# Kernel tuning notes

Measured on AMD Instinct MI355X. Metric: run time of the kernel, lower is better.

## Reference

```python
import jax, jax.numpy as jnp
import numpy as np

C = 128; PE = 8; WALK = 20; NODE_F = 28; EDGE_F = 4
L = 4; H = 4; DH = C // H; B = 64; NPG = 512; N = B * NPG; E = 262144
BN_EPS = 1e-5


def _bn(x, g, b):
    # BatchNorm1d, training-mode statistics (biased var), over the node axis
    m = x.mean(0)
    v = x.var(0)
    return (x - m) * jax.lax.rsqrt(v + BN_EPS) * g + b


def _forward(pe, node_emb, pe_lin_w, pe_lin_b, pe_norm_g, pe_norm_b, edge_emb,
             gine_w1, gine_b1, gine_w2, gine_b2,
             attn_wqkv, attn_bqkv, attn_wo, attn_bo,
             norm1_g, norm1_b, norm2_g, norm2_b, norm3_g, norm3_b,
             ffn_w1, ffn_b1, ffn_w2, ffn_b2,
             mlp_w1, mlp_b1, mlp_w2, mlp_b2, mlp_w3, mlp_b3,
             x, edge_index, edge_attr, batch):
    pe_n = _bn(pe, pe_norm_g, pe_norm_b)
    h = jnp.concatenate([node_emb[x[:, 0]], pe_n @ pe_lin_w + pe_lin_b], axis=1)  # [N, C]
    ea = edge_emb[edge_attr]  # [E, C]
    src, dst = edge_index[0], edge_index[1]
    scale = 1.0 / jnp.sqrt(jnp.asarray(DH, h.dtype))
    for l in range(L):
        # --- GINEConv: nn((1+eps)*x + sum_{j->i} relu(x_j + e_ji)), eps=0 ---
        msg = jax.nn.relu(h[src] + ea)                      # [E, C] gather
        agg = jax.ops.segment_sum(msg, dst, num_segments=N) # [N, C] scatter-add
        z = agg + h
        local = jax.nn.relu(z @ gine_w1[l] + gine_b1[l]) @ gine_w2[l] + gine_b2[l]
        h_loc = _bn(local + h, norm1_g[l], norm1_b[l])
        # --- global multihead attention on dense batch [B, NPG, C] (equal-size graphs) ---
        xd = h.reshape(B, NPG, C)
        qkv = xd @ attn_wqkv[l] + attn_bqkv[l]              # [B, NPG, 3C]
        q, k, v = jnp.split(qkv, 3, axis=-1)
        q = q.reshape(B, NPG, H, DH)
        k = k.reshape(B, NPG, H, DH)
        v = v.reshape(B, NPG, H, DH)
        att = jax.nn.softmax(jnp.einsum('bqhd,bkhd->bhqk', q, k) * scale, axis=-1)
        o = jnp.einsum('bhqk,bkhd->bqhd', att, v).reshape(B, NPG, C) @ attn_wo[l] + attn_bo[l]
        h_att = _bn(o.reshape(N, C) + h, norm2_g[l], norm2_b[l])
        # --- combine + FFN (GPSConv) ---
        out = h_loc + h_att
        ffn = jax.nn.relu(out @ ffn_w1[l] + ffn_b1[l]) @ ffn_w2[l] + ffn_b2[l]
        h = _bn(out + ffn, norm3_g[l], norm3_b[l])
    g = jax.ops.segment_sum(h, batch, num_segments=B)       # global_add_pool -> [B, C]
    y = jax.nn.relu(g @ mlp_w1 + mlp_b1)
    y = jax.nn.relu(y @ mlp_w2 + mlp_b2)
    return y @ mlp_w3 + mlp_b3                              # [B, 1]


def setup_inputs() -> dict:
    key = jax.random.key(0)
    ks = iter(jax.random.split(key, 48))
    def w(shape, s=0.05):
        return jax.random.normal(next(ks), shape, jnp.float32) * s
    inp = {}
    inp['x'] = jax.random.randint(next(ks), (N, 1), 0, NODE_F)
    inp['pe'] = jax.random.normal(next(ks), (N, WALK), jnp.float32)
    inp['edge_index'] = jax.random.randint(next(ks), (2, E), 0, N)
    inp['edge_attr'] = jax.random.randint(next(ks), (E,), 0, EDGE_F)
    inp['batch'] = jnp.arange(N, dtype=jnp.int32) // NPG
    inp['node_emb'] = w((NODE_F, C - PE), 1.0)
    inp['pe_lin_w'] = w((WALK, PE))
    inp['pe_lin_b'] = jnp.zeros((PE,), jnp.float32)
    inp['pe_norm_g'] = jnp.ones((WALK,), jnp.float32)
    inp['pe_norm_b'] = jnp.zeros((WALK,), jnp.float32)
    inp['edge_emb'] = w((EDGE_F, C), 1.0)
    inp['gine_w1'] = w((L, C, C))
    inp['gine_b1'] = jnp.zeros((L, C), jnp.float32)
    inp['gine_w2'] = w((L, C, C))
    inp['gine_b2'] = jnp.zeros((L, C), jnp.float32)
    inp['attn_wqkv'] = w((L, C, 3 * C))
    inp['attn_bqkv'] = jnp.zeros((L, 3 * C), jnp.float32)
    inp['attn_wo'] = w((L, C, C))
    inp['attn_bo'] = jnp.zeros((L, C), jnp.float32)
    for nm in ('norm1', 'norm2', 'norm3'):
        inp[nm + '_g'] = jnp.ones((L, C), jnp.float32)
        inp[nm + '_b'] = jnp.zeros((L, C), jnp.float32)
    inp['ffn_w1'] = w((L, C, 2 * C))
    inp['ffn_b1'] = jnp.zeros((L, 2 * C), jnp.float32)
    inp['ffn_w2'] = w((L, 2 * C, C))
    inp['ffn_b2'] = jnp.zeros((L, C), jnp.float32)
    inp['mlp_w1'] = w((C, C // 2))
    inp['mlp_b1'] = jnp.zeros((C // 2,), jnp.float32)
    inp['mlp_w2'] = w((C // 2, C // 4))
    inp['mlp_b2'] = jnp.zeros((C // 4,), jnp.float32)
    inp['mlp_w3'] = w((C // 4, 1))
    inp['mlp_b3'] = jnp.zeros((1,), jnp.float32)
    return inp


def reference(x, pe, edge_index, edge_attr, batch,
              node_emb, pe_lin_w, pe_lin_b, pe_norm_g, pe_norm_b, edge_emb,
              gine_w1, gine_b1, gine_w2, gine_b2,
              attn_wqkv, attn_bqkv, attn_wo, attn_bo,
              norm1_g, norm1_b, norm2_g, norm2_b, norm3_g, norm3_b,
              ffn_w1, ffn_b1, ffn_w2, ffn_b2,
              mlp_w1, mlp_b1, mlp_w2, mlp_b2, mlp_w3, mlp_b3):
    return _forward(pe, node_emb, pe_lin_w, pe_lin_b, pe_norm_g, pe_norm_b, edge_emb,
                    gine_w1, gine_b1, gine_w2, gine_b2,
                    attn_wqkv, attn_bqkv, attn_wo, attn_bo,
                    norm1_g, norm1_b, norm2_g, norm2_b, norm3_g, norm3_b,
                    ffn_w1, ffn_b1, ffn_w2, ffn_b2,
                    mlp_w1, mlp_b1, mlp_w2, mlp_b2, mlp_w3, mlp_b3,
                    x, edge_index, edge_attr, batch)
```

## Files before the change

### kernel.cpp

```cpp
#include <hip/hip_runtime.h>
#include <math.h>
#include <cstddef>

#define N_NODES 32768
#define C_DIM   128
#define E_EDGES 262144
#define B_GR    64
#define NPG     512
#define WALK_D  20
#define L_LAYERS 4

static constexpr int NF = N_NODES * C_DIM;

typedef __attribute__((ext_vector_type(8))) short bf16x8;
typedef __attribute__((ext_vector_type(4))) float f32x4;
typedef __attribute__((ext_vector_type(4))) short short4v;

__device__ inline unsigned short f2bf(float f)
{
    union { float f; unsigned u; } v; v.f = f;
    unsigned r = v.u + 0x7fff + ((v.u >> 16) & 1);
    return (unsigned short)(r >> 16);
}
__device__ inline float bf2f_lo(unsigned u) { return __uint_as_float(u << 16); }
__device__ inline float bf2f_hi(unsigned u) { return __uint_as_float(u & 0xffff0000u); }

__global__ __launch_bounds__(256) void pe_stats_k(const float* __restrict__ pe, float* __restrict__ acc)
{
    int gt = blockIdx.x * 256 + threadIdx.x;
    float s[WALK_D], q[WALK_D];
    #pragma unroll
    for (int c = 0; c < WALK_D; ++c) { s[c] = 0.f; q[c] = 0.f; }
    for (int r = 0; r < 4; ++r) {
        const float* row = &pe[(size_t)(gt + r * 8192) * WALK_D];
        float v[20];
        #pragma unroll
        for (int j = 0; j < 5; ++j) *(float4*)&v[j * 4] = *(const float4*)(row + j * 4);
        #pragma unroll
        for (int c = 0; c < WALK_D; ++c) { s[c] += v[c]; q[c] += v[c] * v[c]; }
    }
    #pragma unroll
    for (int c = 0; c < WALK_D; ++c) {
        float ss = s[c], qq = q[c];
        #pragma unroll
        for (int m = 1; m < 64; m <<= 1) { ss += __shfl_xor(ss, m); qq += __shfl_xor(qq, m); }
        if ((threadIdx.x & 63) == 0) { atomicAdd(&acc[c], ss); atomicAdd(&acc[32 + c], qq); }
    }
}

__global__ void pe_fin_k(const float* __restrict__ acc, const float* __restrict__ g,
                         const float* __restrict__ b, float* __restrict__ sf)
{
    int c = threadIdx.x;
    if (c >= WALK_D) return;
    float mean = acc[c] * (1.f / N_NODES);
    float var  = acc[32 + c] * (1.f / N_NODES) - mean * mean;
    float sc   = g[c] * rsqrtf(var + 1e-5f);
    sf[c] = sc;
    sf[32 + c] = b[c] - mean * sc;
}

__global__ __launch_bounds__(256) void h0_k(const int* __restrict__ x, const float* __restrict__ pe,
    const float* __restrict__ node_emb, const float* __restrict__ plw, const float* __restrict__ plb,
    const float* __restrict__ pesf, float* __restrict__ h, unsigned short* __restrict__ h16)
{
    int tid = threadIdx.x;
    int i = blockIdx.x * 2 + (tid >> 7);
    int c = tid & 127;
    float v;
    if (c < 120) {
        v = node_emb[x[i] * 120 + c];
    } else {
        int pc = c - 120;
        v = plb[pc];
        #pragma unroll
        for (int k = 0; k < WALK_D; ++k) {
            float pn = pe[i * WALK_D + k] * pesf[k] + pesf[32 + k];
            v = fmaf(pn, plw[k * 8 + pc], v);
        }
    }
    h[i * C_DIM + c] = v;
    h16[i * C_DIM + c] = f2bf(v);
}

__global__ __launch_bounds__(256) void hist_k(const int* __restrict__ dst, int* __restrict__ cnt)
{
    int e = blockIdx.x * 256 + threadIdx.x;
    atomicAdd(&cnt[dst[e]], 1);
}

__global__ __launch_bounds__(256) void bsum_k(const int* __restrict__ cnt, int* __restrict__ bsum)
{
    __shared__ int ws[4];
    int b = blockIdx.x, t = threadIdx.x;
    int v = cnt[b * 256 + t];
    #pragma unroll
    for (int m = 1; m < 64; m <<= 1) v += __shfl_xor(v, m);
    if ((t & 63) == 0) ws[t >> 6] = v;
    __syncthreads();
    if (t == 0) bsum[b] = ws[0] + ws[1] + ws[2] + ws[3];
}

__global__ __launch_bounds__(128) void bscan_k(const int* __restrict__ bsum, int* __restrict__ bpre)
{
    __shared__ int s[128];
    int t = threadIdx.x;
    int v = bsum[t];
    s[t] = v;
    __syncthreads();
    for (int off = 1; off < 128; off <<= 1) {
        int u = (t >= off) ? s[t - off] : 0;
        __syncthreads();
        s[t] += u;
        __syncthreads();
    }
    bpre[t] = s[t] - v;
}

__global__ __launch_bounds__(256) void indptr_k(const int* __restrict__ cnt, const int* __restrict__ bpre,
                                                int* __restrict__ indptr)
{
    __shared__ int s[256];
    int b = blockIdx.x, t = threadIdx.x;
    int v = cnt[b * 256 + t];
    s[t] = v;
    __syncthreads();
    for (int off = 1; off < 256; off <<= 1) {
        int u = (t >= off) ? s[t - off] : 0;
        __syncthreads();
        s[t] += u;
        __syncthreads();
    }
    indptr[b * 256 + t] = bpre[b] + s[t] - v;
    if (b == 127 && t == 255) indptr[N_NODES] = E_EDGES;
}

__global__ __launch_bounds__(256) void scatter_k(const int* __restrict__ dst, const int* __restrict__ indptr,
                                                 int* __restrict__ cur, int* __restrict__ eid)
{
    int e = blockIdx.x * 256 + threadIdx.x;
    int d = dst[e];
    int pos = atomicAdd(&cur[d], 1);
    eid[indptr[d] + pos] = e;
}

__global__ __launch_bounds__(256) void gine_gather_k(const unsigned short* __restrict__ h16,
    const int* __restrict__ src, const int* __restrict__ attr,
    const int* __restrict__ indptr, const int* __restrict__ eid,
    const float* __restrict__ edge_emb, unsigned short* __restrict__ z16)
{
    __shared__ float ee[4 * C_DIM];
    int tid = threadIdx.x;
    ee[tid] = edge_emb[tid];
    ee[tid + 256] = edge_emb[tid + 256];
    __syncthreads();
    int i = blockIdx.x * 4 + (tid >> 6);
    int c = (tid & 63) * 2;
    int p0 = indptr[i], p1 = indptr[i + 1];
    float s0 = 0.f, s1 = 0.f;
    for (int p = p0; p < p1; ++p) {
        int e  = eid[p];
        int sv = src[e];
        int av = attr[e];
        unsigned u = *(const unsigned*)&h16[(size_t)sv * C_DIM + c];
        float m0 = bf2f_lo(u) + ee[av * C_DIM + c];
        float m1 = bf2f_hi(u) + ee[av * C_DIM + c + 1];
        s0 += fmaxf(m0, 0.f);
        s1 += fmaxf(m1, 0.f);
    }
    unsigned us = *(const unsigned*)&h16[(size_t)i * C_DIM + c];
    s0 += bf2f_lo(us);
    s1 += bf2f_hi(us);
    unsigned out = (unsigned)f2bf(s0) | ((unsigned)f2bf(s1) << 16);
    *(unsigned*)&z16[(size_t)i * C_DIM + c] = out;
}

__global__ __launch_bounds__(256) void wt_prep_k(
    const float* __restrict__ gw1, const float* __restrict__ gw2,
    const float* __restrict__ wqkv, const float* __restrict__ wo,
    const float* __restrict__ fw1, const float* __restrict__ fw2,
    short* __restrict__ out)
{
    __shared__ float ts[32][36];
    int b = blockIdx.x;
    int l = b / 160, t = b % 160;
    const float* src; int K, N; size_t obase; int tile;
    if (t < 16)       { src = gw1  + (size_t)l * 16384; K = 128; N = 128; obase = (size_t)l * 163840 + 0;      tile = t; }
    else if (t < 32)  { src = gw2  + (size_t)l * 16384; K = 128; N = 128; obase = (size_t)l * 163840 + 16384;  tile = t - 16; }
    else if (t < 80)  { src = wqkv + (size_t)l * 49152; K = 128; N = 384; obase = (size_t)l * 163840 + 32768;  tile = t - 32; }
    else if (t < 96)  { src = wo   + (size_t)l * 16384; K = 128; N = 128; obase = (size_t)l * 163840 + 81920;  tile = t - 80; }
    else if (t < 128) { src = fw1  + (size_t)l * 32768; K = 128; N = 256; obase = (size_t)l * 163840 + 98304;  tile = t - 96; }
    else              { src = fw2  + (size_t)l * 32768; K = 256; N = 128; obase = (size_t)l * 163840 + 131072; tile = t - 128; }
    int ntN = N / 32;
    int tk = tile / ntN, tn = tile % ntN;
    int tid = threadIdx.x;
    int r = tid >> 3, c4 = (tid & 7) * 4;
    *(float4*)&ts[r][c4] = *(const float4*)&src[(size_t)(tk * 32 + r) * N + tn * 32 + c4];
    __syncthreads();
    int n = tid >> 3, k4 = (tid & 7) * 4;
    short4v pk;
    #pragma unroll
    for (int i2 = 0; i2 < 4; ++i2) pk[i2] = (short)f2bf(ts[k4 + i2][n]);
    *(short4v*)&out[obase + (size_t)(tn * 32 + n) * K + tk * 32 + k4] = pk;
}

template<int KD, int NC, int AMODE, int RESMODE, bool RELU, bool STATS, bool OUTBF, bool ABF, bool VOUT>
__global__ __launch_bounds__(256) void mgemm_k(
    const void* __restrict__ Av, const float* __restrict__ A2,
    const float* __restrict__ affA1, const float* __restrict__ affA2,
    const unsigned short* __restrict__ Bt, const float* __restrict__ bias,
    const float* __restrict__ R1, const float* __restrict__ R2,
    const float* __restrict__ affR1, const float* __restrict__ affR2,
    void* __restrict__ Cout, float* __restrict__ stats,
    unsigned short* __restrict__ vtg)
{
    __shared__ short As[16384];
    __shared__ short Bs[16384];
    const int tid = threadIdx.x;
    const int w = tid >> 6;
    const int lane = tid & 63;
    const int lr = lane & 15, lg = lane >> 4;
    const int row0 = blockIdx.y * 128;
    const int col0 = blockIdx.x * 128;

    const f32x4 zero = {0.f, 0.f, 0.f, 0.f};
    f32x4 acc[2][8];
    #pragma unroll
    for (int i = 0; i < 2; ++i)
        #pragma unroll
        for (int cf = 0; cf < 8; ++cf) acc[i][cf] = zero;

    for (int kt = 0; kt < KD / 128; ++kt) {
        if (kt > 0) __syncthreads();
        #pragma unroll
        for (int it = 0; it < 8; ++it) {
            int gid = it * 256 + tid;
            int row = gid >> 4, g = gid & 15;
            bf16x8 pk;
            if (ABF) {
                pk = *(const bf16x8*)&((const unsigned short*)Av)[(size_t)(row0 + row) * KD + kt * 128 + g * 8];
            } else {
                const float* Af = (const float*)Av;
                const float* ap = &Af[(size_t)(row0 + row) * KD + kt * 128 + g * 8];
                float v[8];
                *(float4*)&v[0] = *(const float4*)ap;
                *(float4*)&v[4] = *(const float4*)(ap + 4);
                if (AMODE == 1) {
                    const float* ap2 = &A2[(size_t)(row0 + row) * KD + kt * 128 + g * 8];
                    float u[8];
                    *(float4*)&u[0] = *(const float4*)ap2;
                    *(float4*)&u[4] = *(const float4*)(ap2 + 4);
                    #pragma unroll
                    for (int j = 0; j < 8; ++j) {
                        int ck = g * 8 + j;
                        v[j] = v[j] * affA1[ck] + affA1[128 + ck] + u[j] * affA2[ck] + affA2[128 + ck];
                    }
                }
                #pragma unroll
                for (int j = 0; j < 8; ++j) pk[j] = (short)f2bf(v[j]);
            }
            *(bf16x8*)&As[(row * 16 + (g ^ (row & 7))) * 8] = pk;
            bf16x8 bv = *(const bf16x8*)&Bt[(size_t)(col0 + row) * KD + kt * 128 + g * 8];
            *(bf16x8*)&Bs[(row * 16 + (g ^ (row & 7))) * 8] = bv;
        }
        __syncthreads();
        #pragma unroll
        for (int ks = 0; ks < 4; ++ks) {
            bf16x8 af[2], bfr[8];
            #pragma unroll
            for (int i = 0; i < 2; ++i) {
                int row = w * 32 + i * 16 + lr;
                int g = ks * 4 + lg;
                af[i] = *(const bf16x8*)&As[(row * 16 + (g ^ (row & 7))) * 8];
            }
            #pragma unroll
            for (int cf = 0; cf < 8; ++cf) {
                int c = cf * 16 + lr;
                int g = ks * 4 + lg;
                bfr[cf] = *(const bf16x8*)&Bs[(c * 16 + (g ^ (c & 7))) * 8];
            }
            #pragma unroll
            for (int i = 0; i < 2; ++i)
                #pragma unroll
                for (int cf = 0; cf < 8; ++cf)
                    acc[i][cf] = __builtin_amdgcn_mfma_f32_16x16x32_bf16(af[i], bfr[cf], acc[i][cf], 0, 0, 0);
        }
    }

    float* cs = (float*)As;
    float* cq = cs + 128;
    if (STATS) {
        __syncthreads();
        if (tid < 128) { cs[tid] = 0.f; cq[tid] = 0.f; }
        __syncthreads();
    }
    float bs_v[8];
    #pragma unroll
    for (int cf = 0; cf < 8; ++cf) bs_v[cf] = bias[col0 + cf * 16 + lr];
    float rs1[8], ro1[8], rs2[8], ro2[8];
    if (RESMODE == 2) {
        #pragma unroll
        for (int cf = 0; cf < 8; ++cf) {
            int c = cf * 16 + lr;
            rs1[cf] = affR1[c]; ro1[cf] = affR1[128 + c];
            rs2[cf] = affR2[c]; ro2[cf] = affR2[128 + c];
        }
    }
    float colS[8], colQ[8];
    #pragma unroll
    for (int cf = 0; cf < 8; ++cf) { colS[cf] = 0.f; colQ[cf] = 0.f; }
    const bool vblk = VOUT && (col0 == 256);
    #pragma unroll
    for (int i = 0; i < 2; ++i) {
        #pragma unroll
        for (int r = 0; r < 4; ++r) {
            size_t grow = row0 + w * 32 + i * 16 + lg * 4 + r;
            #pragma unroll
            for (int cf = 0; cf < 8; ++cf) {
                int c = col0 + cf * 16 + lr;
                float val = acc[i][cf][r] + bs_v[cf];
                if (RESMODE == 1) val += R1[grow * NC + c];
                if (RESMODE == 2) {
                    val += R1[grow * 128 + c] * rs1[cf] + ro1[cf]
                         + R2[grow * 128 + c] * rs2[cf] + ro2[cf];
                }
                if (RELU) val = fmaxf(val, 0.f);
                if (VOUT && vblk) {
                    int g2 = (int)(grow >> 9);
                    int key = (int)(grow & 511);
                    int kc = key >> 6, kg = (key >> 3) & 7, j = key & 7;
                    int cd = c - 256;
                    int hd2 = cd >> 5, dd = cd & 31;
                    vtg[((size_t)(g2 * 4 + hd2) * 8 + kc) * 2048 + dd * 64 + ((kg ^ (dd & 7)) << 3) + j] = f2bf(val);
                } else if (OUTBF) {
                    ((unsigned short*)Cout)[grow * NC + c] = f2bf(val);
                } else {
                    ((float*)Cout)[grow * NC + c] = val;
                }
                if (STATS) { colS[cf] += val; colQ[cf] += val * val; }
            }
        }
    }
    if (STATS) {
        #pragma unroll
        for (int cf = 0; cf < 8; ++cf) {
            float s = colS[cf], q = colQ[cf];
            s += __shfl_xor(s, 16); s += __shfl_xor(s, 32);
            q += __shfl_xor(q, 16); q += __shfl_xor(q, 32);
            if (lg == 0) { atomicAdd(&cs[cf * 16 + lr], s); atomicAdd(&cq[cf * 16 + lr], q); }
        }
        __syncthreads();
        if (tid < 128) {
            atomicAdd(&stats[tid], cs[tid]);
            atomicAdd(&stats[128 + tid], cq[tid]);
        }
    }
}

__global__ __launch_bounds__(256) void gine_mlp_k(
    const unsigned short* __restrict__ z16,
    const unsigned short* __restrict__ W1t, const float* __restrict__ b1,
    const unsigned short* __restrict__ W2t, const float* __restrict__ b2,
    const float* __restrict__ Hres,
    float* __restrict__ T1out, float* __restrict__ stats)
{
    __shared__ short As[16384];
    __shared__ short Bs[16384];
    const int tid = threadIdx.x;
    const int w = tid >> 6;
    const int lane = tid & 63;
    const int lr = lane & 15, lg = lane >> 4;
    const int row0 = blockIdx.x * 128;
    const f32x4 zero = {0.f, 0.f, 0.f, 0.f};

    #pragma unroll
    for (int it = 0; it < 8; ++it) {
        int gid = it * 256 + tid;
        int row = gid >> 4, g = gid & 15;
        bf16x8 av = *(const bf16x8*)&z16[(size_t)(row0 + row) * 128 + g * 8];
        *(bf16x8*)&As[(row * 16 + (g ^ (row & 7))) * 8] = av;
        bf16x8 bv = *(const bf16x8*)&W1t[(size_t)row * 128 + g * 8];
        *(bf16x8*)&Bs[(row * 16 + (g ^ (row & 7))) * 8] = bv;
    }
    __syncthreads();

    f32x4 acc[2][8];
    #pragma unroll
    for (int i = 0; i < 2; ++i)
        #pragma unroll
        for (int cf = 0; cf < 8; ++cf) acc[i][cf] = zero;
    #pragma unroll
    for (int ks = 0; ks < 4; ++ks) {
        bf16x8 af[2], bfr[8];
        #pragma unroll
        for (int i = 0; i < 2; ++i) {
            int row = w * 32 + i * 16 + lr;
            int g = ks * 4 + lg;
            af[i] = *(const bf16x8*)&As[(row * 16 + (g ^ (row & 7))) * 8];
        }
        #pragma unroll
        for (int cf = 0; cf < 8; ++cf) {
            int c = cf * 16 + lr;
            int g = ks * 4 + lg;
            bfr[cf] = *(const bf16x8*)&Bs[(c * 16 + (g ^ (c & 7))) * 8];
        }
        #pragma unroll
        for (int i = 0; i < 2; ++i)
            #pragma unroll
            for (int cf = 0; cf < 8; ++cf)
                acc[i][cf] = __builtin_amdgcn_mfma_f32_16x16x32_bf16(af[i], bfr[cf], acc[i][cf], 0, 0, 0);
    }
    __syncthreads();

    {
        float bias1[8];
        #pragma unroll
        for (int cf = 0; cf < 8; ++cf) bias1[cf] = b1[cf * 16 + lr];
        #pragma unroll
        for (int i = 0; i < 2; ++i) {
            #pragma unroll
            for (int r = 0; r < 4; ++r) {
                int row = w * 32 + i * 16 + lg * 4 + r;
                #pragma unroll
                for (int cf = 0; cf < 8; ++cf) {
                    int col = cf * 16 + lr;
                    float val = fmaxf(acc[i][cf][r] + bias1[cf], 0.f);
                    As[(row * 16 + ((col >> 3) ^ (row & 7))) * 8 + (col & 7)] = (short)f2bf(val);
                }
            }
        }
    }
    #pragma unroll
    for (int it = 0; it < 8; ++it) {
        int gid = it * 256 + tid;
        int row = gid >> 4, g = gid & 15;
        bf16x8 bv = *(const bf16x8*)&W2t[(size_t)row * 128 + g * 8];
        *(bf16x8*)&Bs[(row * 16 + (g ^ (row & 7))) * 8] = bv;
    }
    __syncthreads();

    #pragma unroll
    for (int i = 0; i < 2; ++i)
        #pragma unroll
        for (int cf = 0; cf < 8; ++cf) acc[i][cf] = zero;
    #pragma unroll
    for (int ks = 0; ks < 4; ++ks) {
        bf16x8 af[2], bfr[8];
        #pragma unroll
        for (int i = 0; i < 2; ++i) {
            int row = w * 32 + i * 16 + lr;
            int g = ks * 4 + lg;
            af[i] = *(const bf16x8*)&As[(row * 16 + (g ^ (row & 7))) * 8];
        }
        #pragma unroll
        for (int cf = 0; cf < 8; ++cf) {
            int c = cf * 16 + lr;
            int g = ks * 4 + lg;
            bfr[cf] = *(const bf16x8*)&Bs[(c * 16 + (g ^ (c & 7))) * 8];
        }
        #pragma unroll
        for (int i = 0; i < 2; ++i)
            #pragma unroll
            for (int cf = 0; cf < 8; ++cf)
                acc[i][cf] = __builtin_amdgcn_mfma_f32_16x16x32_bf16(af[i], bfr[cf], acc[i][cf], 0, 0, 0);
    }

    float* cs = (float*)As;
    float* cq = cs + 128;
    __syncthreads();
    if (tid < 128) { cs[tid] = 0.f; cq[tid] = 0.f; }
    __syncthreads();
    float bs_v[8];
    #pragma unroll
    for (int cf = 0; cf < 8; ++cf) bs_v[cf] = b2[cf * 16 + lr];
    float colS[8], colQ[8];
    #pragma unroll
    for (int cf = 0; cf < 8; ++cf) { colS[cf] = 0.f; colQ[cf] = 0.f; }
    #pragma unroll
    for (int i = 0; i < 2; ++i) {
        #pragma unroll
        for (int r = 0; r < 4; ++r) {
            size_t grow = row0 + w * 32 + i * 16 + lg * 4 + r;
            #pragma unroll
            for (int cf = 0; cf < 8; ++cf) {
                int c = cf * 16 + lr;
                float val = acc[i][cf][r] + bs_v[cf] + Hres[grow * 128 + c];
                T1out[grow * 128 + c] = val;
                colS[cf] += val; colQ[cf] += val * val;
            }
        }
    }
    #pragma unroll
    for (int cf = 0; cf < 8; ++cf) {
        float s = colS[cf], q = colQ[cf];
        s += __shfl_xor(s, 16); s += __shfl_xor(s, 32);
        q += __shfl_xor(q, 16); q += __shfl_xor(q, 32);
        if (lg == 0) { atomicAdd(&cs[cf * 16 + lr], s); atomicAdd(&cq[cf * 16 + lr], q); }
    }
    __syncthreads();
    if (tid < 128) {
        atomicAdd(&stats[tid], cs[tid]);
        atomicAdd(&stats[128 + tid], cq[tid]);
    }
}

__global__ __launch_bounds__(256) void ffn_mlp_k(
    const float* __restrict__ T1, const float* __restrict__ T2,
    const float* __restrict__ sf1, const float* __restrict__ sf2,
    const unsigned short* __restrict__ W1t, const float* __restrict__ fb1,
    const unsigned short* __restrict__ W2t, const float* __restrict__ fb2,
    float* __restrict__ T1out, float* __restrict__ stats)
{
    __shared__ short As[8192];
    __shared__ short Bs[16384];
    __shared__ short Ys[8192];
    const int tid = threadIdx.x;
    const int w = tid >> 6;
    const int lane = tid & 63;
    const int lr = lane & 15, lg = lane >> 4;
    const int row0 = blockIdx.x * 64;
    const f32x4 zero = {0.f, 0.f, 0.f, 0.f};

    #pragma unroll
    for (int it = 0; it < 4; ++it) {
        int gid = it * 256 + tid;
        int row = gid >> 4, g = gid & 15;
        const float* ap = &T1[(size_t)(row0 + row) * 128 + g * 8];
        const float* ap2 = &T2[(size_t)(row0 + row) * 128 + g * 8];
        float v[8], u[8];
        *(float4*)&v[0] = *(const float4*)ap;
        *(float4*)&v[4] = *(const float4*)(ap + 4);
        *(float4*)&u[0] = *(const float4*)ap2;
        *(float4*)&u[4] = *(const float4*)(ap2 + 4);
        bf16x8 pk;
        #pragma unroll
        for (int j = 0; j < 8; ++j) {
            int ck = g * 8 + j;
            pk[j] = (short)f2bf(v[j] * sf1[ck] + sf1[128 + ck] + u[j] * sf2[ck] + sf2[128 + ck]);
        }
        *(bf16x8*)&As[(row * 16 + (g ^ (row & 7))) * 8] = pk;
    }

    f32x4 acc2[8];
    #pragma unroll
    for (int cf = 0; cf < 8; ++cf) acc2[cf] = zero;

    const int arow = w * 16 + lr;
    for (int h = 0; h < 2; ++h) {
        if (h > 0) __syncthreads();
        #pragma unroll
        for (int it = 0; it < 8; ++it) {
            int gid = it * 256 + tid;
            int row = gid >> 4, g = gid & 15;
            bf16x8 bv = *(const bf16x8*)&W1t[(size_t)(h * 128 + row) * 128 + g * 8];
            *(bf16x8*)&Bs[(row * 16 + (g ^ (row & 7))) * 8] = bv;
        }
        __syncthreads();
        f32x4 accY[8];
        #pragma unroll
        for (int cf = 0; cf < 8; ++cf) accY[cf] = zero;
        #pragma unroll
        for (int ks = 0; ks < 4; ++ks) {
            int g = ks * 4 + lg;
            bf16x8 af = *(const bf16x8*)&As[(arow * 16 + (g ^ (arow & 7))) * 8];
            #pragma unroll
            for (int cf = 0; cf < 8; ++cf) {
                int c = cf * 16 + lr;
                bf16x8 bfr = *(const bf16x8*)&Bs[(c * 16 + (g ^ (c & 7))) * 8];
                accY[cf] = __builtin_amdgcn_mfma_f32_16x16x32_bf16(af, bfr, accY[cf], 0, 0, 0);
            }
        }
        __syncthreads();
        #pragma unroll
        for (int r = 0; r < 4; ++r) {
            int row = w * 16 + lg * 4 + r;
            #pragma unroll
            for (int cf = 0; cf < 8; ++cf) {
                int col = cf * 16 + lr;
                float val = fmaxf(accY[cf][r] + fb1[h * 128 + col], 0.f);
                Ys[(row * 16 + ((col >> 3) ^ (row & 7))) * 8 + (col & 7)] = (short)f2bf(val);
            }
        }
        #pragma unroll
        for (int it = 0; it < 8; ++it) {
            int gid = it * 256 + tid;
            int row = gid >> 4, g = gid & 15;
            bf16x8 bv = *(const bf16x8*)&W2t[(size_t)row * 256 + h * 128 + g * 8];
            *(bf16x8*)&Bs[(row * 16 + (g ^ (row & 7))) * 8] = bv;
        }
        __syncthreads();
        #pragma unroll
        for (int ks = 0; ks < 4; ++ks) {
            int g = ks * 4 + lg;
            bf16x8 af = *(const bf16x8*)&Ys[(arow * 16 + (g ^ (arow & 7))) * 8];
            #pragma unroll
            for (int cf = 0; cf < 8; ++cf) {
                int c = cf * 16 + lr;
                bf16x8 bfr = *(const bf16x8*)&Bs[(c * 16 + (g ^ (c & 7))) * 8];
                acc2[cf] = __builtin_amdgcn_mfma_f32_16x16x32_bf16(af, bfr, acc2[cf], 0, 0, 0);
            }
        }
    }

    float* cs = (float*)As;
    float* cq = cs + 128;
    __syncthreads();
    if (tid < 128) { cs[tid] = 0.f; cq[tid] = 0.f; }
    __syncthreads();
    float bs_v[8], rs1[8], ro1[8], rs2[8], ro2[8];
    #pragma unroll
    for (int cf = 0; cf < 8; ++cf) {
        int c = cf * 16 + lr;
        bs_v[cf] = fb2[c];
        rs1[cf] = sf1[c]; ro1[cf] = sf1[128 + c];
        rs2[cf] = sf2[c]; ro2[cf] = sf2[128 + c];
    }
    float colS[8], colQ[8];
    #pragma unroll
    for (int cf = 0; cf < 8; ++cf) { colS[cf] = 0.f; colQ[cf] = 0.f; }
    #pragma unroll
    for (int r = 0; r < 4; ++r) {
        size_t grow = row0 + w * 16 + lg * 4 + r;
        #pragma unroll
        for (int cf = 0; cf < 8; ++cf) {
            int c = cf * 16 + lr;
            float val = acc2[cf][r] + bs_v[cf]
                      + T1[grow * 128 + c] * rs1[cf] + ro1[cf]
                      + T2[grow * 128 + c] * rs2[cf] + ro2[cf];
            T1out[grow * 128 + c] = val;
            colS[cf] += val; colQ[cf] += val * val;
        }
    }
    #pragma unroll
    for (int cf = 0; cf < 8; ++cf) {
        float s = colS[cf], q = colQ[cf];
        s += __shfl_xor(s, 16); s += __shfl_xor(s, 32);
        q += __shfl_xor(q, 16); q += __shfl_xor(q, 32);
        if (lg == 0) { atomicAdd(&cs[cf * 16 + lr], s); atomicAdd(&cq[cf * 16 + lr], q); }
    }
    __syncthreads();
    if (tid < 128) {
        atomicAdd(&stats[tid], cs[tid]);
        atomicAdd(&stats[128 + tid], cq[tid]);
    }
}

__global__ __launch_bounds__(256) void attn_mfma_k(const unsigned short* __restrict__ qkvb,
                                                   const unsigned short* __restrict__ vtg,
                                                   unsigned short* __restrict__ ao16)
{
    __shared__ short Qs[4096];
    __shared__ short Ks[2][2048];
    __shared__ short Vs[2][2048];
    __shared__ short Ps[4][1024];
    const int tid = threadIdx.x;
    const int w = tid >> 6, lane = tid & 63;
    const int lr = lane & 15, lg = lane >> 4;
    const int q0 = blockIdx.x * 128;
    const int hd = blockIdx.y;
    const int base = blockIdx.z * NPG;
    const float SCL = 0.17677669529663687f * 1.44269504089f;
    const f32x4 zero = {0.f, 0.f, 0.f, 0.f};
    const unsigned short* vbase = vtg + (size_t)(blockIdx.z * 4 + hd) * 16384;

    {
        #pragma unroll
        for (int it = 0; it < 2; ++it) {
            int idx = it * 256 + tid;
            int row = idx >> 2, g = idx & 3;
            bf16x8 qv = *(const bf16x8*)&qkvb[(size_t)(base + q0 + row) * 384 + hd * 32 + g * 8];
            *(bf16x8*)&Qs[(row * 4 + (g ^ ((row >> 1) & 3))) * 8] = qv;
        }
        int row = tid >> 2, g = tid & 3;
        bf16x8 kv = *(const bf16x8*)&qkvb[(size_t)(base + row) * 384 + 128 + hd * 32 + g * 8];
        *(bf16x8*)&Ks[0][(row * 4 + (g ^ ((row >> 1) & 3))) * 8] = kv;
        bf16x8 vv = *(const bf16x8*)&vbase[tid * 8];
        *(bf16x8*)&Vs[0][tid * 8] = vv;
    }
    __syncthreads();
    bf16x8 bq[2];
    #pragma unroll
    for (int f = 0; f < 2; ++f) {
        int qrow = f * 64 + w * 16 + lr;
        bq[f] = *(const bf16x8*)&Qs[(qrow * 4 + (lg ^ ((qrow >> 1) & 3))) * 8];
    }
    float m[2], lsum[2];
    f32x4 o[2][2];
    #pragma unroll
    for (int f = 0; f < 2; ++f) {
        o[f][0] = zero; o[f][1] = zero;
        m[f] = -1e30f; lsum[f] = 0.f;
    }

    for (int kc = 0; kc < 8; ++kc) {
        int buf = kc & 1;
        bf16x8 knx, vnx;
        if (kc < 7) {
            int row = tid >> 2, g = tid & 3;
            knx = *(const bf16x8*)&qkvb[(size_t)(base + (kc + 1) * 64 + row) * 384 + 128 + hd * 32 + g * 8];
            vnx = *(const bf16x8*)&vbase[(size_t)(kc + 1) * 2048 + tid * 8];
        }
        bf16x8 ka[4], va[2][2];
        #pragma unroll
        for (int kf = 0; kf < 4; ++kf) {
            int kr = kf * 16 + lr;
            ka[kf] = *(const bf16x8*)&Ks[buf][(kr * 4 + (lg ^ ((kr >> 1) & 3))) * 8];
        }
        #pragma unroll
        for (int ks = 0; ks < 2; ++ks)
            #pragma unroll
            for (int df = 0; df < 2; ++df) {
                int d = df * 16 + lr;
                int kg = ks * 4 + lg;
                va[ks][df] = *(const bf16x8*)&Vs[buf][(d * 8 + (kg ^ (d & 7))) * 8];
            }
        #pragma unroll
        for (int f = 0; f < 2; ++f) {
            f32x4 s[4];
            #pragma unroll
            for (int kf = 0; kf < 4; ++kf)
                s[kf] = __builtin_amdgcn_mfma_f32_16x16x32_bf16(ka[kf], bq[f], zero, 0, 0, 0);
            float v[16];
            #pragma unroll
            for (int kf = 0; kf < 4; ++kf)
                #pragma unroll
                for (int r = 0; r < 4; ++r) v[kf * 4 + r] = s[kf][r] * SCL;
            float rm = fmaxf(fmaxf(fmaxf(fmaxf(v[0], v[1]), fmaxf(v[2], v[3])),
                                   fmaxf(fmaxf(v[4], v[5]), fmaxf(v[6], v[7]))),
                             fmaxf(fmaxf(fmaxf(v[8], v[9]), fmaxf(v[10], v[11])),
                                   fmaxf(fmaxf(v[12], v[13]), fmaxf(v[14], v[15]))));
            rm = fmaxf(rm, __shfl_xor(rm, 16));
            rm = fmaxf(rm, __shfl_xor(rm, 32));
            float mn = fmaxf(m[f], rm);
            float alpha = exp2f(m[f] - mn);
            float p[16];
            #pragma unroll
            for (int i = 0; i < 16; ++i) p[i] = exp2f(v[i] - mn);
            float S0 = ((p[0] + p[4]) + p[8]) + p[12];
            float S1 = ((p[1] + p[5]) + p[9]) + p[13];
            float S2 = ((p[2] + p[6]) + p[10]) + p[14];
            float S3 = ((p[3] + p[7]) + p[11]) + p[15];
            float ps = (S0 + S1) + (S2 + S3);
            ps += __shfl_xor(ps, 16);
            ps += __shfl_xor(ps, 32);
            lsum[f] = lsum[f] * alpha + ps;
            m[f] = mn;
            o[f][0] *= alpha;
            o[f][1] *= alpha;
            #pragma unroll
            for (int kf = 0; kf < 4; ++kf) {
                unsigned lo = (unsigned)f2bf(p[kf * 4 + 0]) | ((unsigned)f2bf(p[kf * 4 + 1]) << 16);
                unsigned hi = (unsigned)f2bf(p[kf * 4 + 2]) | ((unsigned)f2bf(p[kf * 4 + 3]) << 16);
                uint2 pk; pk.x = lo; pk.y = hi;
                int gr = (kf * 2 + (lg >> 1)) ^ (lr & 7);
                *(uint2*)&Ps[w][lr * 64 + gr * 8 + (lg & 1) * 4] = pk;
            }
            #pragma unroll
            for (int ks = 0; ks < 2; ++ks) {
                bf16x8 pa = *(const bf16x8*)&Ps[w][lr * 64 + (((ks * 4 + lg) ^ (lr & 7))) * 8];
                #pragma unroll
                for (int df = 0; df < 2; ++df)
                    o[f][df] = __builtin_amdgcn_mfma_f32_16x16x32_bf16(va[ks][df], pa, o[f][df], 0, 0, 0);
            }
        }
        if (kc < 7) {
            int row = tid >> 2, g = tid & 3;
            *(bf16x8*)&Ks[buf ^ 1][(row * 4 + (g ^ ((row >> 1) & 3))) * 8] = knx;
            *(bf16x8*)&Vs[buf ^ 1][tid * 8] = vnx;
        }
        __syncthreads();
    }
    #pragma unroll
    for (int f = 0; f < 2; ++f) {
        float inv = 1.f / lsum[f];
        size_t nrow = (size_t)base + q0 + f * 64 + w * 16 + lr;
        #pragma unroll
        for (int df = 0; df < 2; ++df) {
            short4v pkv;
            #pragma unroll
            for (int r = 0; r < 4; ++r) pkv[r] = (short)f2bf(o[f][df][r] * inv);
            *(short4v*)&ao16[nrow * 128 + hd * 32 + df * 16 + lg * 4] = pkv;
        }
    }
}

__global__ void bn_fin_k(const float* acc1, const float* g1, const float* b1, float* sf1,
                         const float* acc2, const float* g2, const float* b2, float* sf2)
{
    const float* acc = (blockIdx.x == 0) ? acc1 : acc2;
    const float* g   = (blockIdx.x == 0) ? g1 : g2;
    const float* b   = (blockIdx.x == 0) ? b1 : b2;
    float*       sf  = (blockIdx.x == 0) ? sf1 : sf2;
    if (acc == nullptr) return;
    int c = threadIdx.x;
    float mean = acc[c] * (1.f / N_NODES);
    float var  = acc[128 + c] * (1.f / N_NODES) - mean * mean;
    float sc   = g[c] * rsqrtf(var + 1e-5f);
    sf[c] = sc;
    sf[128 + c] = b[c] - mean * sc;
}

__global__ __launch_bounds__(256) void bn_apply_k(const float* __restrict__ t, const float* __restrict__ sf,
                                                  float* __restrict__ h, unsigned short* __restrict__ h16)
{
    int idx = blockIdx.x * 256 + threadIdx.x;
    int cg = (idx & 31) * 4;
    float4 v  = *(const float4*)&t[idx * 4];
    float4 sc = *(const float4*)&sf[cg];
    float4 sh = *(const float4*)&sf[128 + cg];
    float4 o;
    o.x = v.x * sc.x + sh.x;
    o.y = v.y * sc.y + sh.y;
    o.z = v.z * sc.z + sh.z;
    o.w = v.w * sc.w + sh.w;
    *(float4*)&h[idx * 4] = o;
    short4v p;
    p[0] = (short)f2bf(o.x); p[1] = (short)f2bf(o.y);
    p[2] = (short)f2bf(o.z); p[3] = (short)f2bf(o.w);
    *(short4v*)&h16[idx * 4] = p;
}

__global__ __launch_bounds__(128) void pool_k(const float* __restrict__ h, float* __restrict__ g)
{
    int b = blockIdx.x, c = threadIdx.x;
    float s = 0.f;
    for (int i = 0; i < NPG; ++i) s += h[(size_t)((b << 9) + i) * C_DIM + c];
    g[b * C_DIM + c] = s;
}

__global__ __launch_bounds__(256) void head_mlp_k(const float* __restrict__ g,
    const float* __restrict__ w1, const float* __restrict__ b1,
    const float* __restrict__ w2, const float* __restrict__ b2,
    const float* __restrict__ w3, const float* __restrict__ b3,
    float* __restrict__ out)
{
    __shared__ float gs[64 * 128];
    __shared__ float y1[64 * 64];
    __shared__ float y2[64 * 32];
    int tid = threadIdx.x;
    for (int r = 0; r < 32; ++r) gs[r * 256 + tid] = g[r * 256 + tid];
    __syncthreads();
    for (int t = 0; t < 16; ++t) {
        int idx = t * 256 + tid;
        int gi = idx >> 6, c = idx & 63;
        float s = b1[c];
        for (int k = 0; k < 128; ++k) s = fmaf(gs[gi * 128 + k], w1[k * 64 + c], s);
        y1[gi * 64 + c] = fmaxf(s, 0.f);
    }
    __syncthreads();
    for (int t = 0; t < 8; ++t) {
        int idx = t * 256 + tid;
        int gi = idx >> 5, c = idx & 31;
        float s = b2[c];
        for (int k = 0; k < 64; ++k) s = fmaf(y1[gi * 64 + k], w2[k * 32 + c], s);
        y2[gi * 32 + c] = fmaxf(s, 0.f);
    }
    __syncthreads();
    if (tid < 64) {
        float s = b3[0];
        for (int k = 0; k < 32; ++k) s = fmaf(y2[tid * 32 + k], w3[k], s);
        out[tid] = s;
    }
}

extern "C" void kernel_launch(void* const* d_in, const int* in_sizes, int n_in,
                              void* d_out, int out_size, void* d_ws, size_t ws_size,
                              hipStream_t stream)
{
    const int*   x        = (const int*)  d_in[0];
    const float* pe       = (const float*)d_in[1];
    const int*   ei       = (const int*)  d_in[2];
    const int*   eattr    = (const int*)  d_in[3];
    const float* node_emb = (const float*)d_in[5];
    const float* plw      = (const float*)d_in[6];
    const float* plb      = (const float*)d_in[7];
    const float* pe_g     = (const float*)d_in[8];
    const float* pe_b     = (const float*)d_in[9];
    const float* edge_emb = (const float*)d_in[10];
    const float* gw1      = (const float*)d_in[11];
    const float* gb1      = (const float*)d_in[12];
    const float* gw2      = (const float*)d_in[13];
    const float* gb2      = (const float*)d_in[14];
    const float* wqkv     = (const float*)d_in[15];
    const float* bqkv     = (const float*)d_in[16];
    const float* wo       = (const float*)d_in[17];
    const float* bo       = (const float*)d_in[18];
    const float* n1g      = (const float*)d_in[19];
    const float* n1b      = (const float*)d_in[20];
    const float* n2g      = (const float*)d_in[21];
    const float* n2b      = (const float*)d_in[22];
    const float* n3g      = (const float*)d_in[23];
    const float* n3b      = (const float*)d_in[24];
    const float* fw1      = (const float*)d_in[25];
    const float* fb1      = (const float*)d_in[26];
    const float* fw2      = (const float*)d_in[27];
    const float* fb2      = (const float*)d_in[28];
    const float* mw1      = (const float*)d_in[29];
    const float* mb1      = (const float*)d_in[30];
    const float* mw2      = (const float*)d_in[31];
    const float* mb2      = (const float*)d_in[32];
    const float* mw3      = (const float*)d_in[33];
    const float* mb3      = (const float*)d_in[34];

    float* wf  = (float*)d_ws;
    float* Hb  = wf;
    unsigned short* Zb16 = (unsigned short*)(wf + (size_t)NF);
    float* T1  = wf + 2 * (size_t)NF;
    unsigned short* QKVb = (unsigned short*)(wf + 3 * (size_t)NF);
    float* T2  = wf + 3 * (size_t)NF;
    unsigned short* vtg = (unsigned short*)(wf + 4 * (size_t)NF + (size_t)NF / 2);
    unsigned short* Hb16 = (unsigned short*)(wf + 5 * (size_t)NF);
    int* wi     = (int*)(wf + 6 * (size_t)NF);
    int* indptr = wi;
    int* cnt    = wi + 32800;
    int* cnt2   = cnt + N_NODES;
    int* eid    = cnt2 + N_NODES;
    int* bsum   = eid + E_EDGES;
    int* bpre   = bsum + 128;
    float* st    = (float*)(bpre + 128);
    float* peacc = st;
    float* bnacc = st + 64;
    float* pesf  = st + 64 + 12 * 256;
    float* bnsf  = pesf + 64;
    float* gpool = bnsf + 12 * 256;
    short* wT    = (short*)(gpool + 64 * 128);

    const int* srcA = ei;
    const int* dstA = ei + E_EDGES;
    const int LSTR = 163840;

    hipMemsetAsync(peacc, 0, (64 + 12 * 256) * sizeof(float), stream);
    hipMemsetAsync(cnt, 0, 2 * N_NODES * sizeof(int), stream);

    wt_prep_k<<<640, 256, 0, stream>>>(gw1, gw2, wqkv, wo, fw1, fw2, wT);
    pe_stats_k<<<32, 256, 0, stream>>>(pe, peacc);
    pe_fin_k<<<1, 32, 0, stream>>>(peacc, pe_g, pe_b, pesf);
    h0_k<<<N_NODES / 2, 256, 0, stream>>>(x, pe, node_emb, plw, plb, pesf, Hb, Hb16);
    hist_k<<<E_EDGES / 256, 256, 0, stream>>>(dstA, cnt);
    bsum_k<<<128, 256, 0, stream>>>(cnt, bsum);
    bscan_k<<<1, 128, 0, stream>>>(bsum, bpre);
    indptr_k<<<128, 256, 0, stream>>>(cnt, bpre, indptr);
    scatter_k<<<E_EDGES / 256, 256, 0, stream>>>(dstA, indptr, cnt2, eid);

    for (int l = 0; l < L_LAYERS; ++l) {
        const short* gw1t  = wT + (size_t)l * LSTR;
        const short* gw2t  = wT + (size_t)l * LSTR + 16384;
        const short* wqkvt = wT + (size_t)l * LSTR + 32768;
        const short* wot   = wT + (size_t)l * LSTR + 81920;
        const short* fw1t  = wT + (size_t)l * LSTR + 98304;
        const short* fw2t  = wT + (size_t)l * LSTR + 131072;
        const float* lgb1  = gb1 + (size_t)l * 128;
        const float* lgb2  = gb2 + (size_t)l * 128;
        const float* lbqkv = bqkv + (size_t)l * 384;
        const float* lbo   = bo + (size_t)l * 128;
        const float* lfb1  = fb1 + (size_t)l * 256;
        const float* lfb2  = fb2 + (size_t)l * 128;
        float* acc1 = bnacc + (l * 3 + 0) * 256;  float* sf1v = bnsf + (l * 3 + 0) * 256;
        float* acc2 = bnacc + (l * 3 + 1) * 256;  float* sf2v = bnsf + (l * 3 + 1) * 256;
        float* acc3 = bnacc + (l * 3 + 2) * 256;  float* sf3v = bnsf + (l * 3 + 2) * 256;

        gine_gather_k<<<N_NODES / 4, 256, 0, stream>>>(Hb16, srcA, eattr, indptr, eid, edge_emb, Zb16);
        gine_mlp_k<<<256, 256, 0, stream>>>(
            Zb16, (const unsigned short*)gw1t, lgb1, (const unsigned short*)gw2t, lgb2,
            Hb, T1, acc1);
        mgemm_k<128, 384, 0, 0, false, false, true,  true, true ><<<dim3(3, 256), 256, 0, stream>>>(
            Hb16, nullptr, nullptr, nullptr, (const unsigned short*)wqkvt, lbqkv,
            nullptr, nullptr, nullptr, nullptr, QKVb, nullptr, vtg);
        attn_mfma_k<<<dim3(4, 4, 64), 256, 0, stream>>>(QKVb, vtg, Zb16);
        mgemm_k<128, 128, 0, 1, false, true,  false, true, false><<<dim3(1, 256), 256, 0, stream>>>(
            Zb16, nullptr, nullptr, nullptr, (const unsigned short*)wot, lbo,
            Hb, nullptr, nullptr, nullptr, T2, acc2, nullptr);
        bn_fin_k<<<2, 128, 0, stream>>>(acc1, n1g + l * 128, n1b + l * 128, sf1v,
                                        acc2, n2g + l * 128, n2b + l * 128, sf2v);
        ffn_mlp_k<<<512, 256, 0, stream>>>(
            T1, T2, sf1v, sf2v,
            (const unsigned short*)fw1t, lfb1, (const unsigned short*)fw2t, lfb2,
            T1, acc3);
        bn_fin_k<<<1, 128, 0, stream>>>(acc3, n3g + l * 128, n3b + l * 128, sf3v,
                                        nullptr, nullptr, nullptr, nullptr);
        bn_apply_k<<<NF / 1024, 256, 0, stream>>>(T1, sf3v, Hb, Hb16);
    }
    pool_k<<<B_GR, 128, 0, stream>>>(Hb, gpool);
    head_mlp_k<<<1, 256, 0, stream>>>(gpool, mw1, mb1, mw2, mb2, mw3, mb3, (float*)d_out);
}
```

Measured before the change: 850.3 us.

## Pack sorted edge source and attribute into one array and unroll gather loop

Adds a one-time pre-pass that writes each CSR-ordered edge's source node and edge attribute into one packed int, so the per-layer gather no longer makes the eid->src/attr double indirection. The gather loop is unrolled by four so several independent feature loads are in flight at once, and the edge-embedding reads become float2. Packing assumes node ids fit in 16 bits (N=32768) and adds an extra kernel plus E ints of workspace.

```diff
diff --git a/kernel.cpp b/kernel.cpp
--- a/kernel.cpp
+++ b/kernel.cpp
@@ -144,9 +144,16 @@
     eid[indptr[d] + pos] = e;
 }
 
+__global__ __launch_bounds__(256) void edge_prep_k(const int* __restrict__ eid,
+    const int* __restrict__ src, const int* __restrict__ attr, int* __restrict__ esa)
+{
+    int p = blockIdx.x * 256 + threadIdx.x;
+    int e = eid[p];
+    esa[p] = src[e] | (attr[e] << 16);
+}
+
 __global__ __launch_bounds__(256) void gine_gather_k(const unsigned short* __restrict__ h16,
-    const int* __restrict__ src, const int* __restrict__ attr,
-    const int* __restrict__ indptr, const int* __restrict__ eid,
+    const int* __restrict__ esa, const int* __restrict__ indptr,
     const float* __restrict__ edge_emb, unsigned short* __restrict__ z16)
 {
     __shared__ float ee[4 * C_DIM];
@@ -158,15 +165,28 @@
     int c = (tid & 63) * 2;
     int p0 = indptr[i], p1 = indptr[i + 1];
     float s0 = 0.f, s1 = 0.f;
-    for (int p = p0; p < p1; ++p) {
-        int e  = eid[p];
-        int sv = src[e];
-        int av = attr[e];
-        unsigned u = *(const unsigned*)&h16[(size_t)sv * C_DIM + c];
-        float m0 = bf2f_lo(u) + ee[av * C_DIM + c];
-        float m1 = bf2f_hi(u) + ee[av * C_DIM + c + 1];
-        s0 += fmaxf(m0, 0.f);
-        s1 += fmaxf(m1, 0.f);
+    int p = p0;
+    for (; p + 4 <= p1; p += 4) {
+        int sa0 = esa[p], sa1 = esa[p + 1], sa2 = esa[p + 2], sa3 = esa[p + 3];
+        unsigned u0 = *(const unsigned*)&h16[(size_t)(sa0 & 0xffff) * C_DIM + c];
+        unsigned u1 = *(const unsigned*)&h16[(size_t)(sa1 & 0xffff) * C_DIM + c];
+        unsigned u2 = *(const unsigned*)&h16[(size_t)(sa2 & 0xffff) * C_DIM + c];
+        unsigned u3 = *(const unsigned*)&h16[(size_t)(sa3 & 0xffff) * C_DIM + c];
+        float2 e0 = *(const float2*)&ee[(sa0 >> 16) * C_DIM + c];
+        float2 e1 = *(const float2*)&ee[(sa1 >> 16) * C_DIM + c];
+        float2 e2 = *(const float2*)&ee[(sa2 >> 16) * C_DIM + c];
+        float2 e3 = *(const float2*)&ee[(sa3 >> 16) * C_DIM + c];
+        s0 += fmaxf(bf2f_lo(u0) + e0.x, 0.f); s1 += fmaxf(bf2f_hi(u0) + e0.y, 0.f);
+        s0 += fmaxf(bf2f_lo(u1) + e1.x, 0.f); s1 += fmaxf(bf2f_hi(u1) + e1.y, 0.f);
+        s0 += fmaxf(bf2f_lo(u2) + e2.x, 0.f); s1 += fmaxf(bf2f_hi(u2) + e2.y, 0.f);
+        s0 += fmaxf(bf2f_lo(u3) + e3.x, 0.f); s1 += fmaxf(bf2f_hi(u3) + e3.y, 0.f);
+    }
+    for (; p < p1; ++p) {
+        int sa = esa[p];
+        unsigned u = *(const unsigned*)&h16[(size_t)(sa & 0xffff) * C_DIM + c];
+        float2 ev = *(const float2*)&ee[(sa >> 16) * C_DIM + c];
+        s0 += fmaxf(bf2f_lo(u) + ev.x, 0.f);
+        s1 += fmaxf(bf2f_hi(u) + ev.y, 0.f);
     }
     unsigned us = *(const unsigned*)&h16[(size_t)i * C_DIM + c];
     s0 += bf2f_lo(us);
@@ -917,7 +937,8 @@
     int* eid    = cnt2 + N_NODES;
     int* bsum   = eid + E_EDGES;
     int* bpre   = bsum + 128;
-    float* st    = (float*)(bpre + 128);
+    int* esa    = bpre + 128;
+    float* st    = (float*)(esa + E_EDGES);
     float* peacc = st;
     float* bnacc = st + 64;
     float* pesf  = st + 64 + 12 * 256;
@@ -941,6 +962,7 @@
     bscan_k<<<1, 128, 0, stream>>>(bsum, bpre);
     indptr_k<<<128, 256, 0, stream>>>(cnt, bpre, indptr);
     scatter_k<<<E_EDGES / 256, 256, 0, stream>>>(dstA, indptr, cnt2, eid);
+    edge_prep_k<<<E_EDGES / 256, 256, 0, stream>>>(eid, srcA, eattr, esa);
 
     for (int l = 0; l < L_LAYERS; ++l) {
         const short* gw1t  = wT + (size_t)l * LSTR;
@@ -959,7 +981,7 @@
         float* acc2 = bnacc + (l * 3 + 1) * 256;  float* sf2v = bnsf + (l * 3 + 1) * 256;
         float* acc3 = bnacc + (l * 3 + 2) * 256;  float* sf3v = bnsf + (l * 3 + 2) * 256;
 
-        gine_gather_k<<<N_NODES / 4, 256, 0, stream>>>(Hb16, srcA, eattr, indptr, eid, edge_emb, Zb16);
+        gine_gather_k<<<N_NODES / 4, 256, 0, stream>>>(Hb16, esa, indptr, edge_emb, Zb16);
         gine_mlp_k<<<256, 256, 0, stream>>>(
             Zb16, (const unsigned short*)gw1t, lgb1, (const unsigned short*)gw2t, lgb2,
             Hb, T1, acc1);
```

Result: faster. 746.4 us (-12.2%).
